# Kernel tuning notes

Measured on AMD Instinct MI355X. Metric: run time of the kernel, lower is better.

Reference implementation:

```python
import jax, jax.numpy as jnp
import numpy as np

B, S, H = 4, 2048, 1024
NH, HD = 16, 64  # num heads, head dim

def setup_inputs() -> dict:
    key = jax.random.key(0)
    ks = jax.random.split(key, 4)
    scale = 1.0 / np.sqrt(H)
    return {
        "hidden_states": jax.random.normal(ks[0], (B, S, H), dtype=jnp.float32),
        "attention_mask": jnp.zeros((B, 1, 1, S), dtype=jnp.float32),
        "wq": jax.random.normal(ks[1], (H, H), dtype=jnp.float32) * scale,
        "bq": jnp.zeros((H,), dtype=jnp.float32),
        "wk": jax.random.normal(ks[2], (H, H), dtype=jnp.float32) * scale,
        "bk": jnp.zeros((H,), dtype=jnp.float32),
        "wv": jax.random.normal(ks[3], (H, H), dtype=jnp.float32) * scale,
        "bv": jnp.zeros((H,), dtype=jnp.float32),
    }

def _split_heads(x):
    # [B,S,H] -> [B,NH,S,HD]
    return x.reshape(B, S, NH, HD).transpose(0, 2, 1, 3)

def reference(hidden_states, attention_mask, wq, bq, wk, bk, wv, bv):
    # torch F.linear: x @ W^T + b
    q = _split_heads(hidden_states @ wq.T + bq)
    k = _split_heads(hidden_states @ wk.T + bk)
    v = _split_heads(hidden_states @ wv.T + bv)
    scores = jnp.einsum("bhqd,bhkd->bhqk", q, k) / np.sqrt(HD)
    scores = scores + attention_mask  # additive mask, broadcast [B,1,1,S]
    probs = jax.nn.softmax(scores, axis=-1)  # dropout p=0.0 (eval)
    ctx = jnp.einsum("bhqk,bhkd->bhqd", probs, v)
    # [B,NH,S,HD] -> [B,S,H]
    return ctx.transpose(0, 2, 1, 3).reshape(B, S, H)
```

## Files before the change

### kernel.cpp

```cpp
#include <hip/hip_runtime.h>

typedef unsigned short u16;
typedef unsigned int u32;
typedef __bf16 bf16;
typedef bf16 bf16x8 __attribute__((ext_vector_type(8)));
typedef float f32x4 __attribute__((ext_vector_type(4)));
typedef float f32x16 __attribute__((ext_vector_type(16)));
typedef u16 u16x8 __attribute__((ext_vector_type(8)));
typedef u16 u16x4 __attribute__((ext_vector_type(4)));
typedef u32 u32x4 __attribute__((ext_vector_type(4)));

#define B_ 4
#define S_ 2048
#define H_ 1024
#define NH_ 16
#define HD_ 64
#define M_TOT (B_ * S_)
#define N_TOT (3 * H_)

#if __has_builtin(__builtin_amdgcn_exp2f)
#define EXP2(x) __builtin_amdgcn_exp2f(x)
#else
static __device__ __forceinline__ float exp2_hw(float x) {
    float r; asm("v_exp_f32 %0, %1" : "=v"(r) : "v"(x)); return r;
}
#define EXP2(x) exp2_hw(x)
#endif

__device__ __forceinline__ u16 f2bf(float f) {
    union { float f; unsigned u; } v; v.f = f;
    unsigned r = v.u + 0x7FFFu + ((v.u >> 16) & 1u);
    return (u16)(r >> 16);
}

__device__ __forceinline__ u32 cvt_pk_bf16(float a, float b) {
    u32 r;
    asm("v_cvt_pk_bf16_f32 %0, %1, %2" : "=v"(r) : "v"(a), "v"(b));
    return r;
}
__device__ __forceinline__ void perm32swap(u32& a, u32& b) {
    asm volatile("v_permlane32_swap_b32 %0, %1" : "+v"(a), "+v"(b));
}
__device__ __forceinline__ void gload16(const void* g, void* l) {
    __builtin_amdgcn_global_load_lds(
        (const __attribute__((address_space(1))) void*)g,
        (__attribute__((address_space(3))) void*)l, 16, 0, 0);
}
__device__ __forceinline__ void wait_vm0() {
    asm volatile("s_waitcnt vmcnt(0)" ::: "memory");
}

__global__ __launch_bounds__(256) void cvt_bf16(const float* __restrict__ src,
                                                u16* __restrict__ dst, int n4) {
    int i = blockIdx.x * blockDim.x + threadIdx.x;
    int stride = gridDim.x * blockDim.x;
    for (; i < n4; i += stride) {
        float4 v = ((const float4*)src)[i];
        u16x4 o = { f2bf(v.x), f2bf(v.y), f2bf(v.z), f2bf(v.w) };
        *(u16x4*)&dst[i * 4] = o;
    }
}

__global__ __launch_bounds__(256) void qkv_gemm(
    const u16* __restrict__ X, const u16* __restrict__ W,
    const float* __restrict__ bq, const float* __restrict__ bk, const float* __restrict__ bv,
    u16* __restrict__ Q, u16* __restrict__ Ko, u16* __restrict__ Vt) {
    __shared__ __align__(16) u16 As[2][128 * 32];
    __shared__ __align__(16) u16 Bs[2][128 * 32];

    const int tid = threadIdx.x;
    const int lane = tid & 63;
    const int wave = tid >> 6;
    const int m0 = blockIdx.y * 128;
    const int n0 = blockIdx.x * 128;
    const int wr = (wave >> 1) * 64;
    const int wc = (wave & 1) * 64;

    f32x4 acc[4][4];
#pragma unroll
    for (int m = 0; m < 4; m++)
#pragma unroll
        for (int n = 0; n < 4; n++) acc[m][n] = (f32x4){0.f, 0.f, 0.f, 0.f};

    const int ci = wave * 64 + lane;
    const int ra = ci >> 2, ca = (ci & 3) * 8;
    const u16* gA0 = &X[(size_t)(m0 + ra) * H_ + ca];
    const u16* gA1 = &X[(size_t)(m0 + ra + 64) * H_ + ca];
    const u16* gB0 = &W[(size_t)(n0 + ra) * H_ + ca];
    const u16* gB1 = &W[(size_t)(n0 + ra + 64) * H_ + ca];
    char* lA0 = (char*)&As[0][0] + wave * 1024;
    char* lB0 = (char*)&Bs[0][0] + wave * 1024;

    const int row_a = lane & 15;
    const int ko = (lane >> 4) * 8;

    gload16(gA0, lA0);
    gload16(gA1, lA0 + 4096);
    gload16(gB0, lB0);
    gload16(gB1, lB0 + 4096);

    for (int k0 = 0; k0 < H_; k0 += 32) {
        const int cur = (k0 >> 5) & 1;
        wait_vm0();
        __builtin_amdgcn_s_barrier();
        if (k0 + 32 < H_) {
            char* dA = lA0 + (cur ^ 1) * 8192;
            char* dB = lB0 + (cur ^ 1) * 8192;
            gload16(gA0 + k0 + 32, dA);
            gload16(gA1 + k0 + 32, dA + 4096);
            gload16(gB0 + k0 + 32, dB);
            gload16(gB1 + k0 + 32, dB + 4096);
        }
        const u16* Ab = &As[cur][0];
        const u16* Bb = &Bs[cur][0];
        bf16x8 a[4], bfr[4];
#pragma unroll
        for (int m = 0; m < 4; m++)
            a[m] = *(const bf16x8*)&Ab[(wr + m * 16 + row_a) * 32 + ko];
#pragma unroll
        for (int n = 0; n < 4; n++)
            bfr[n] = *(const bf16x8*)&Bb[(wc + n * 16 + row_a) * 32 + ko];
#pragma unroll
        for (int m = 0; m < 4; m++)
#pragma unroll
            for (int n = 0; n < 4; n++)
                acc[m][n] = __builtin_amdgcn_mfma_f32_16x16x32_bf16(a[m], bfr[n], acc[m][n], 0, 0, 0);
    }

    const float QS = 0.125f * 1.44269504f;
#pragma unroll
    for (int n = 0; n < 4; n++) {
        int ng = n0 + wc + n * 16 + (lane & 15);
        int which = ng >> 10;
        int nn = ng & 1023;
        const float* bp = (which == 0) ? bq : (which == 1) ? bk : bv;
        float bias = bp[nn];
        float scale = (which == 0) ? QS : 1.0f;
        int h = nn >> 6, d = nn & 63;
#pragma unroll
        for (int m = 0; m < 4; m++) {
            int mg0 = m0 + wr + m * 16 + (lane >> 4) * 4;
            if (which == 2) {
                u16x4 pack;
#pragma unroll
                for (int j = 0; j < 4; j++) pack[j] = f2bf(acc[m][n][j] + bias);
                int bb = mg0 >> 11, s = mg0 & 2047;
                *(u16x4*)&Vt[((((size_t)bb * NH_ + h) * HD_) + d) * S_ + s] = pack;
            } else {
                u16* dst = (which == 0) ? Q : Ko;
#pragma unroll
                for (int j = 0; j < 4; j++) {
                    int mg = mg0 + j;
                    int bb = mg >> 11, s = mg & 2047;
                    float v = (acc[m][n][j] + bias) * scale;
                    dst[((((size_t)bb * NH_ + h) * S_) + s) * HD_ + d] = f2bf(v);
                }
            }
        }
    }
}

#define KVB 64
#define NT_ (S_ / KVB)

__global__ __launch_bounds__(256, 4) void attn(
    const u16* __restrict__ Q, const u16* __restrict__ K, const u16* __restrict__ Vt,
    const float* __restrict__ mask, float* __restrict__ out) {
    const int head = blockIdx.y;
    const int b = head >> 4, h = head & 15;
    const int q0 = blockIdx.x * 128;
    const int tid = threadIdx.x;
    const int lane = tid & 63;
    const int wave = tid >> 6;
    const int l31 = lane & 31;
    const int hi = lane >> 5;

    const u16* Qh = Q + (size_t)head * S_ * HD_;
    const u16* Kh = K + (size_t)head * S_ * HD_;
    const u16* Vh = Vt + (size_t)head * HD_ * S_;

    __shared__ __align__(16) u16 Kl[2][KVB * HD_];
    __shared__ __align__(16) u16 Vl[2][HD_ * KVB];
    __shared__ int snz;

    if (tid == 0) snz = 0;
    __syncthreads();
    {
        int nz = 0;
        const f32x4* m4 = (const f32x4*)(mask + (size_t)b * S_);
        for (int i = tid; i < S_ / 4; i += 256) {
            f32x4 v = m4[i];
            nz |= (v[0] != 0.f) | (v[1] != 0.f) | (v[2] != 0.f) | (v[3] != 0.f);
        }
        if (__any(nz) && lane == 0) atomicOr(&snz, 1);
    }

    bf16x8 qf[4];
    {
        const u16* qp = &Qh[(size_t)(q0 + wave * 32 + l31) * HD_ + hi * 8];
        qf[0] = *(const bf16x8*)(qp);
        qf[1] = *(const bf16x8*)(qp + 16);
        qf[2] = *(const bf16x8*)(qp + 32);
        qf[3] = *(const bf16x8*)(qp + 48);
    }
    __syncthreads();
    const bool mz = (snz == 0);
    const float* mrow = mask + (size_t)b * S_;
    const float LOG2E = 1.44269504f;

    const int c0 = wave * 64 + lane;
    const int c1 = 256 + c0;
    const int r0c = c0 >> 3, r1c = c1 >> 3;
    const u32 s0c = (u32)(((c0 & 7) ^ (r0c & 7)) * 16);
    const u32 s1c = (u32)(((c1 & 7) ^ (r1c & 7)) * 16);
    const char* kS0 = (const char*)Kh + (size_t)r0c * 128 + s0c;
    const char* kS1 = (const char*)Kh + (size_t)r1c * 128 + s1c;
    const char* vS0 = (const char*)Vh + (size_t)r0c * (S_ * 2) + s0c;
    const char* vS1 = (const char*)Vh + (size_t)r1c * (S_ * 2) + s1c;
    char* dK = (char*)&Kl[0][0] + wave * 1024;
    char* dV = (char*)&Vl[0][0] + wave * 1024;

    const u32 swzR = (u32)((l31 & 7) << 4);
    const u32 rowB = (u32)(l31 * 128);

    f32x16 oacc[2];
#pragma unroll
    for (int dh = 0; dh < 2; dh++)
#pragma unroll
        for (int i = 0; i < 16; i++) oacc[dh][i] = 0.f;
    float m = -1e30f, l = 0.f;

    gload16(kS0, dK);
    gload16(kS1, dK + 4096);
    gload16(vS0, dV);
    gload16(vS1, dV + 4096);

    for (int t = 0; t < NT_; ++t) {
        const int kv0 = t * KVB;
        const int cur = t & 1;
        wait_vm0();
        __builtin_amdgcn_s_barrier();
        if (t + 1 < NT_) {
            const size_t kOff = (size_t)(kv0 + KVB) * 128;
            const size_t vOff = (size_t)(kv0 + KVB) * 2;
            char* nK = dK + (cur ^ 1) * 8192;
            char* nV = dV + (cur ^ 1) * 8192;
            gload16(kS0 + kOff, nK);
            gload16(kS1 + kOff, nK + 4096);
            gload16(vS0 + vOff, nV);
            gload16(vS1 + vOff, nV + 4096);
        }
        const char* KB = (const char*)&Kl[cur][0];
        const char* VB = (const char*)&Vl[cur][0];

        f32x16 sc[2];
#pragma unroll
        for (int g = 0; g < 2; g++) {
            f32x16 c;
#pragma unroll
            for (int i = 0; i < 16; i++) c[i] = 0.f;
#pragma unroll
            for (int dk = 0; dk < 4; dk++) {
                bf16x8 kf = *(const bf16x8*)(KB + g * 4096 + rowB +
                                             (((u32)(dk * 32 + hi * 16)) ^ swzR));
                c = __builtin_amdgcn_mfma_f32_32x32x16_bf16(kf, qf[dk], c, 0, 0, 0);
            }
            sc[g] = c;
        }

        if (!mz) {
#pragma unroll
            for (int g = 0; g < 2; g++)
#pragma unroll
                for (int c4 = 0; c4 < 4; c4++) {
                    f32x4 mk = *(const f32x4*)&mrow[kv0 + g * 32 + c4 * 8 + hi * 4];
#pragma unroll
                    for (int e = 0; e < 4; e++) sc[g][c4 * 4 + e] += mk[e] * LOG2E;
                }
        }

        float tm = sc[0][0];
#pragma unroll
        for (int i = 1; i < 16; i++) tm = fmaxf(tm, sc[0][i]);
#pragma unroll
        for (int i = 0; i < 16; i++) tm = fmaxf(tm, sc[1][i]);
        tm = fmaxf(tm, __shfl_xor(tm, 32, 64));
        if (tm > m + 30.f) {
            float fac = EXP2(m - tm);
            l *= fac;
#pragma unroll
            for (int dh = 0; dh < 2; dh++)
#pragma unroll
                for (int i = 0; i < 16; i++) oacc[dh][i] *= fac;
            m = tm;
        }

        float l0 = 0.f, l1 = 0.f, l2 = 0.f, l3 = 0.f;
#pragma unroll
        for (int g = 0; g < 2; g++)
#pragma unroll
            for (int i = 0; i < 16; i += 4) {
                float p0 = EXP2(sc[g][i + 0] - m);
                float p1 = EXP2(sc[g][i + 1] - m);
                float p2 = EXP2(sc[g][i + 2] - m);
                float p3 = EXP2(sc[g][i + 3] - m);
                sc[g][i + 0] = p0; sc[g][i + 1] = p1;
                sc[g][i + 2] = p2; sc[g][i + 3] = p3;
                l0 += p0; l1 += p1; l2 += p2; l3 += p3;
            }
        l += (l0 + l1) + (l2 + l3);

#pragma unroll
        for (int s = 0; s < 4; s++) {
            const int g = s >> 1, r8 = (s & 1) * 8;
            u32 pkA0 = cvt_pk_bf16(sc[g][r8 + 0], sc[g][r8 + 1]);
            u32 pkA1 = cvt_pk_bf16(sc[g][r8 + 2], sc[g][r8 + 3]);
            u32 pkB0 = cvt_pk_bf16(sc[g][r8 + 4], sc[g][r8 + 5]);
            u32 pkB1 = cvt_pk_bf16(sc[g][r8 + 6], sc[g][r8 + 7]);
            perm32swap(pkA0, pkB0);
            perm32swap(pkA1, pkB1);
            union { u32x4 w; bf16x8 v; } pu;
            pu.w = (u32x4){ pkA0, pkA1, pkB0, pkB1 };
            bf16x8 pf = pu.v;
#pragma unroll
            for (int dh = 0; dh < 2; dh++) {
                bf16x8 vf = *(const bf16x8*)(VB + dh * 4096 + rowB +
                                             (((u32)(s * 32 + hi * 16)) ^ swzR));
                oacc[dh] = __builtin_amdgcn_mfma_f32_32x32x16_bf16(vf, pf, oacc[dh], 0, 0, 0);
            }
        }
    }

    float lt = l + __shfl_xor(l, 32, 64);
    float inv = 1.0f / lt;
    const int q = q0 + wave * 32 + l31;
    float* orow = out + ((size_t)b * S_ + q) * H_ + h * HD_;
#pragma unroll
    for (int dh = 0; dh < 2; dh++)
#pragma unroll
        for (int c4 = 0; c4 < 4; c4++) {
            f32x4 v;
#pragma unroll
            for (int e = 0; e < 4; e++) v[e] = oacc[dh][c4 * 4 + e] * inv;
            *(f32x4*)&orow[dh * 32 + c4 * 8 + hi * 4] = v;
        }
}

extern "C" void kernel_launch(void* const* d_in, const int* in_sizes, int n_in,
                              void* d_out, int out_size, void* d_ws, size_t ws_size,
                              hipStream_t stream) {
    const float* hs   = (const float*)d_in[0];
    const float* mask = (const float*)d_in[1];
    const float* wq   = (const float*)d_in[2];
    const float* bq   = (const float*)d_in[3];
    const float* wk   = (const float*)d_in[4];
    const float* bk   = (const float*)d_in[5];
    const float* wv   = (const float*)d_in[6];
    const float* bv   = (const float*)d_in[7];
    float* out = (float*)d_out;

    char* ws = (char*)d_ws;
    u16* Xb = (u16*)ws;
    u16* Wb = (u16*)(ws + 16777216);
    u16* Qb = (u16*)(ws + 23068672);
    u16* Kb = (u16*)(ws + 39845888);
    u16* Vb = (u16*)(ws + 56623104);

    cvt_bf16<<<1024, 256, 0, stream>>>(hs, Xb, (M_TOT * H_) / 4);
    cvt_bf16<<<512, 256, 0, stream>>>(wq, Wb,                (H_ * H_) / 4);
    cvt_bf16<<<512, 256, 0, stream>>>(wk, Wb + H_ * H_,      (H_ * H_) / 4);
    cvt_bf16<<<512, 256, 0, stream>>>(wv, Wb + 2 * H_ * H_,  (H_ * H_) / 4);

    qkv_gemm<<<dim3(N_TOT / 128, M_TOT / 128), 256, 0, stream>>>(
        Xb, Wb, bq, bk, bv, Qb, Kb, Vb);

    attn<<<dim3(S_ / 128, B_ * NH_), 256, 0, stream>>>(Qb, Kb, Vb, mask, out);
}
```

Measured before the change: 220.8 us.

## Merge conversion kernels, enlarge GEMM tile with 32x32 MFMA, 512-thread attention blocks

```diff
diff --git a/kernel.cpp b/kernel.cpp
--- a/kernel.cpp
+++ b/kernel.cpp
@@ -50,110 +50,130 @@
     asm volatile("s_waitcnt vmcnt(0)" ::: "memory");
 }
 
-__global__ __launch_bounds__(256) void cvt_bf16(const float* __restrict__ src,
-                                                u16* __restrict__ dst, int n4) {
+__global__ __launch_bounds__(256) void cvt_all(
+    const float* __restrict__ x, const float* __restrict__ wq,
+    const float* __restrict__ wk, const float* __restrict__ wv,
+    u16* __restrict__ xb, u16* __restrict__ wb) {
+    const int X4 = (M_TOT * H_) / 4;
+    const int W4 = (H_ * H_) / 4;
+    const int total = X4 + 3 * W4;
     int i = blockIdx.x * blockDim.x + threadIdx.x;
     int stride = gridDim.x * blockDim.x;
-    for (; i < n4; i += stride) {
-        float4 v = ((const float4*)src)[i];
+    for (; i < total; i += stride) {
+        const float* src; u16* dst; int off;
+        if (i < X4) { src = x; dst = xb; off = i; }
+        else {
+            int j = i - X4;
+            int w = j >> 18;
+            off = j & (W4 - 1);
+            src = (w == 0) ? wq : (w == 1) ? wk : wv;
+            dst = wb + w * (H_ * H_);
+        }
+        float4 v = ((const float4*)src)[off];
         u16x4 o = { f2bf(v.x), f2bf(v.y), f2bf(v.z), f2bf(v.w) };
-        *(u16x4*)&dst[i * 4] = o;
-    }
-}
-
-__global__ __launch_bounds__(256) void qkv_gemm(
+        *(u16x4*)&dst[off * 4] = o;
+    }
+}
+
+__global__ __launch_bounds__(512, 2) void qkv_gemm(
     const u16* __restrict__ X, const u16* __restrict__ W,
     const float* __restrict__ bq, const float* __restrict__ bk, const float* __restrict__ bv,
     u16* __restrict__ Q, u16* __restrict__ Ko, u16* __restrict__ Vt) {
-    __shared__ __align__(16) u16 As[2][128 * 32];
+    __shared__ __align__(16) u16 As[2][256 * 32];
     __shared__ __align__(16) u16 Bs[2][128 * 32];
 
     const int tid = threadIdx.x;
     const int lane = tid & 63;
     const int wave = tid >> 6;
-    const int m0 = blockIdx.y * 128;
+    const int l31 = lane & 31;
+    const int hi = lane >> 5;
+    const int m0 = blockIdx.y * 256;
     const int n0 = blockIdx.x * 128;
     const int wr = (wave >> 1) * 64;
     const int wc = (wave & 1) * 64;
 
-    f32x4 acc[4][4];
-#pragma unroll
-    for (int m = 0; m < 4; m++)
-#pragma unroll
-        for (int n = 0; n < 4; n++) acc[m][n] = (f32x4){0.f, 0.f, 0.f, 0.f};
-
-    const int ci = wave * 64 + lane;
-    const int ra = ci >> 2, ca = (ci & 3) * 8;
-    const u16* gA0 = &X[(size_t)(m0 + ra) * H_ + ca];
-    const u16* gA1 = &X[(size_t)(m0 + ra + 64) * H_ + ca];
-    const u16* gB0 = &W[(size_t)(n0 + ra) * H_ + ca];
-    const u16* gB1 = &W[(size_t)(n0 + ra + 64) * H_ + ca];
-    char* lA0 = (char*)&As[0][0] + wave * 1024;
-    char* lB0 = (char*)&Bs[0][0] + wave * 1024;
-
-    const int row_a = lane & 15;
-    const int ko = (lane >> 4) * 8;
-
-    gload16(gA0, lA0);
-    gload16(gA1, lA0 + 4096);
-    gload16(gB0, lB0);
-    gload16(gB1, lB0 + 4096);
+    f32x16 acc[2][2];
+#pragma unroll
+    for (int mf = 0; mf < 2; mf++)
+#pragma unroll
+        for (int nf = 0; nf < 2; nf++)
+#pragma unroll
+            for (int i = 0; i < 16; i++) acc[mf][nf][i] = 0.f;
+
+    const int ca = tid;
+    const int raA = ca >> 2, caA = (ca & 3) * 8;
+    const u16* gA0 = &X[(size_t)(m0 + raA) * H_ + caA];
+    const u16* gA1 = &X[(size_t)(m0 + 128 + raA) * H_ + caA];
+    const u16* gB0 = &W[(size_t)(n0 + raA) * H_ + caA];
+    char* lA = (char*)&As[0][0] + wave * 1024;
+    char* lB = (char*)&Bs[0][0] + wave * 1024;
+
+    gload16(gA0, lA);
+    gload16(gA1, lA + 8192);
+    gload16(gB0, lB);
 
     for (int k0 = 0; k0 < H_; k0 += 32) {
         const int cur = (k0 >> 5) & 1;
         wait_vm0();
         __builtin_amdgcn_s_barrier();
         if (k0 + 32 < H_) {
-            char* dA = lA0 + (cur ^ 1) * 8192;
-            char* dB = lB0 + (cur ^ 1) * 8192;
+            char* dA = lA + (cur ^ 1) * 16384;
+            char* dB = lB + (cur ^ 1) * 8192;
             gload16(gA0 + k0 + 32, dA);
-            gload16(gA1 + k0 + 32, dA + 4096);
+            gload16(gA1 + k0 + 32, dA + 8192);
             gload16(gB0 + k0 + 32, dB);
-            gload16(gB1 + k0 + 32, dB + 4096);
         }
         const u16* Ab = &As[cur][0];
         const u16* Bb = &Bs[cur][0];
-        bf16x8 a[4], bfr[4];
-#pragma unroll
-        for (int m = 0; m < 4; m++)
-            a[m] = *(const bf16x8*)&Ab[(wr + m * 16 + row_a) * 32 + ko];
-#pragma unroll
-        for (int n = 0; n < 4; n++)
-            bfr[n] = *(const bf16x8*)&Bb[(wc + n * 16 + row_a) * 32 + ko];
-#pragma unroll
-        for (int m = 0; m < 4; m++)
-#pragma unroll
-            for (int n = 0; n < 4; n++)
-                acc[m][n] = __builtin_amdgcn_mfma_f32_16x16x32_bf16(a[m], bfr[n], acc[m][n], 0, 0, 0);
+        bf16x8 a[2][2], bfr[2][2];
+#pragma unroll
+        for (int mf = 0; mf < 2; mf++)
+#pragma unroll
+            for (int ks = 0; ks < 2; ks++)
+                a[mf][ks] = *(const bf16x8*)&Ab[(wr + mf * 32 + l31) * 32 + ks * 16 + hi * 8];
+#pragma unroll
+        for (int nf = 0; nf < 2; nf++)
+#pragma unroll
+            for (int ks = 0; ks < 2; ks++)
+                bfr[nf][ks] = *(const bf16x8*)&Bb[(wc + nf * 32 + l31) * 32 + ks * 16 + hi * 8];
+#pragma unroll
+        for (int mf = 0; mf < 2; mf++)
+#pragma unroll
+            for (int nf = 0; nf < 2; nf++)
+#pragma unroll
+                for (int ks = 0; ks < 2; ks++)
+                    acc[mf][nf] = __builtin_amdgcn_mfma_f32_32x32x16_bf16(
+                        a[mf][ks], bfr[nf][ks], acc[mf][nf], 0, 0, 0);
     }
 
     const float QS = 0.125f * 1.44269504f;
-#pragma unroll
-    for (int n = 0; n < 4; n++) {
-        int ng = n0 + wc + n * 16 + (lane & 15);
-        int which = ng >> 10;
+    const int which = n0 >> 10;
+    const float* bp = (which == 0) ? bq : (which == 1) ? bk : bv;
+#pragma unroll
+    for (int nf = 0; nf < 2; nf++) {
+        int ng = n0 + wc + nf * 32 + l31;
         int nn = ng & 1023;
-        const float* bp = (which == 0) ? bq : (which == 1) ? bk : bv;
         float bias = bp[nn];
-        float scale = (which == 0) ? QS : 1.0f;
         int h = nn >> 6, d = nn & 63;
 #pragma unroll
-        for (int m = 0; m < 4; m++) {
-            int mg0 = m0 + wr + m * 16 + (lane >> 4) * 4;
-            if (which == 2) {
-                u16x4 pack;
-#pragma unroll
-                for (int j = 0; j < 4; j++) pack[j] = f2bf(acc[m][n][j] + bias);
-                int bb = mg0 >> 11, s = mg0 & 2047;
-                *(u16x4*)&Vt[((((size_t)bb * NH_ + h) * HD_) + d) * S_ + s] = pack;
-            } else {
-                u16* dst = (which == 0) ? Q : Ko;
-#pragma unroll
-                for (int j = 0; j < 4; j++) {
-                    int mg = mg0 + j;
-                    int bb = mg >> 11, s = mg & 2047;
-                    float v = (acc[m][n][j] + bias) * scale;
-                    dst[((((size_t)bb * NH_ + h) * S_) + s) * HD_ + d] = f2bf(v);
+        for (int mf = 0; mf < 2; mf++) {
+#pragma unroll
+            for (int q = 0; q < 4; q++) {
+                int mrow0 = m0 + wr + mf * 32 + 8 * q + 4 * hi;
+                int bb = mrow0 >> 11, s0 = mrow0 & 2047;
+                if (which == 2) {
+                    u16x4 pack;
+#pragma unroll
+                    for (int j = 0; j < 4; j++) pack[j] = f2bf(acc[mf][nf][q * 4 + j] + bias);
+                    *(u16x4*)&Vt[((((size_t)bb * NH_ + h) * HD_) + d) * S_ + s0] = pack;
+                } else {
+                    u16* dst = (which == 0) ? Q : Ko;
+                    float scale = (which == 0) ? QS : 1.0f;
+#pragma unroll
+                    for (int j = 0; j < 4; j++) {
+                        float v = (acc[mf][nf][q * 4 + j] + bias) * scale;
+                        dst[((((size_t)bb * NH_ + h) * S_) + s0 + j) * HD_ + d] = f2bf(v);
+                    }
                 }
             }
         }
@@ -163,12 +183,12 @@
 #define KVB 64
 #define NT_ (S_ / KVB)
 
-__global__ __launch_bounds__(256, 4) void attn(
+__global__ __launch_bounds__(512, 4) void attn(
     const u16* __restrict__ Q, const u16* __restrict__ K, const u16* __restrict__ Vt,
     const float* __restrict__ mask, float* __restrict__ out) {
     const int head = blockIdx.y;
     const int b = head >> 4, h = head & 15;
-    const int q0 = blockIdx.x * 128;
+    const int q0 = blockIdx.x * 256;
     const int tid = threadIdx.x;
     const int lane = tid & 63;
     const int wave = tid >> 6;
@@ -188,7 +208,7 @@
     {
         int nz = 0;
         const f32x4* m4 = (const f32x4*)(mask + (size_t)b * S_);
-        for (int i = tid; i < S_ / 4; i += 256) {
+        for (int i = tid; i < S_ / 4; i += 512) {
             f32x4 v = m4[i];
             nz |= (v[0] != 0.f) | (v[1] != 0.f) | (v[2] != 0.f) | (v[3] != 0.f);
         }
@@ -208,15 +228,10 @@
     const float* mrow = mask + (size_t)b * S_;
     const float LOG2E = 1.44269504f;
 
-    const int c0 = wave * 64 + lane;
-    const int c1 = 256 + c0;
-    const int r0c = c0 >> 3, r1c = c1 >> 3;
-    const u32 s0c = (u32)(((c0 & 7) ^ (r0c & 7)) * 16);
-    const u32 s1c = (u32)(((c1 & 7) ^ (r1c & 7)) * 16);
-    const char* kS0 = (const char*)Kh + (size_t)r0c * 128 + s0c;
-    const char* kS1 = (const char*)Kh + (size_t)r1c * 128 + s1c;
-    const char* vS0 = (const char*)Vh + (size_t)r0c * (S_ * 2) + s0c;
-    const char* vS1 = (const char*)Vh + (size_t)r1c * (S_ * 2) + s1c;
+    const int rc = tid >> 3;
+    const u32 sc16 = (u32)(((tid & 7) ^ (rc & 7)) * 16);
+    const char* kSrc = (const char*)Kh + (size_t)rc * 128 + sc16;
+    const char* vSrc = (const char*)Vh + (size_t)rc * (S_ * 2) + sc16;
     char* dK = (char*)&Kl[0][0] + wave * 1024;
     char* dV = (char*)&Vl[0][0] + wave * 1024;
 
@@ -230,10 +245,8 @@
         for (int i = 0; i < 16; i++) oacc[dh][i] = 0.f;
     float m = -1e30f, l = 0.f;
 
-    gload16(kS0, dK);
-    gload16(kS1, dK + 4096);
-    gload16(vS0, dV);
-    gload16(vS1, dV + 4096);
+    gload16(kSrc, dK);
+    gload16(vSrc, dV);
 
     for (int t = 0; t < NT_; ++t) {
         const int kv0 = t * KVB;
@@ -241,14 +254,8 @@
         wait_vm0();
         __builtin_amdgcn_s_barrier();
         if (t + 1 < NT_) {
-            const size_t kOff = (size_t)(kv0 + KVB) * 128;
-            const size_t vOff = (size_t)(kv0 + KVB) * 2;
-            char* nK = dK + (cur ^ 1) * 8192;
-            char* nV = dV + (cur ^ 1) * 8192;
-            gload16(kS0 + kOff, nK);
-            gload16(kS1 + kOff, nK + 4096);
-            gload16(vS0 + vOff, nV);
-            gload16(vS1 + vOff, nV + 4096);
+            gload16(kSrc + (size_t)(kv0 + KVB) * 128, dK + (cur ^ 1) * 8192);
+            gload16(vSrc + (size_t)(kv0 + KVB) * 2,   dV + (cur ^ 1) * 8192);
         }
         const char* KB = (const char*)&Kl[cur][0];
         const char* VB = (const char*)&Vl[cur][0];
@@ -366,13 +373,10 @@
     u16* Kb = (u16*)(ws + 39845888);
     u16* Vb = (u16*)(ws + 56623104);
 
-    cvt_bf16<<<1024, 256, 0, stream>>>(hs, Xb, (M_TOT * H_) / 4);
-    cvt_bf16<<<512, 256, 0, stream>>>(wq, Wb,                (H_ * H_) / 4);
-    cvt_bf16<<<512, 256, 0, stream>>>(wk, Wb + H_ * H_,      (H_ * H_) / 4);
-    cvt_bf16<<<512, 256, 0, stream>>>(wv, Wb + 2 * H_ * H_,  (H_ * H_) / 4);
-
-    qkv_gemm<<<dim3(N_TOT / 128, M_TOT / 128), 256, 0, stream>>>(
+    cvt_all<<<2048, 256, 0, stream>>>(hs, wq, wk, wv, Xb, Wb);
+
+    qkv_gemm<<<dim3(N_TOT / 128, M_TOT / 256), 512, 0, stream>>>(
         Xb, Wb, bq, bk, bv, Qb, Kb, Vb);
 
-    attn<<<dim3(S_ / 128, B_ * NH_), 256, 0, stream>>>(Qb, Kb, Vb, mask, out);
-}
+    attn<<<dim3(S_ / 256, B_ * NH_), 512, 0, stream>>>(Qb, Kb, Vb, mask, out);
+}
```

After: 200.3 us. -9.3%, faster.
